# Kernel tuning notes

Hardware: AMD Instinct MI355X
Metric: run time of the kernel (lower is better)

Reference implementation:

```python
import jax, jax.numpy as jnp
import numpy as np

N, E, D_IN, D, H = 50000, 600000, 128, 128, 128
NEG_SLOPE = 0.2  # PyG GATConv default


def setup_inputs() -> dict:
    key = jax.random.key(0)
    ks = jax.random.split(key, 10)
    s = 1.0 / np.sqrt(D)
    return {
        "x": jax.random.normal(ks[0], (N, D_IN), jnp.float32),
        "edge_index": jax.random.randint(ks[1], (2, E), 0, N, jnp.int64),
        "h": jax.random.normal(ks[2], (1, N, H), jnp.float32),
        "c": jax.random.normal(ks[3], (1, N, H), jnp.float32),
        "W": jax.random.normal(ks[4], (D_IN, D), jnp.float32) * s,
        "att_src": jax.random.normal(ks[5], (D,), jnp.float32) * s,
        "att_dst": jax.random.normal(ks[6], (D,), jnp.float32) * s,
        "bias_gat": jnp.zeros((D,), jnp.float32),
        "W_ih": jax.random.normal(ks[7], (4 * H, D), jnp.float32) * s,
        "W_hh": jax.random.normal(ks[8], (4 * H, H), jnp.float32) * s,
    }


def _gat_conv(x, edge_index, W, att_src, att_dst, bias_gat):
    n = x.shape[0]
    xs = x @ W  # [N, D]
    # add self loops (PyG default add_self_loops=True)
    loop = jnp.arange(n, dtype=edge_index.dtype)
    src = jnp.concatenate([edge_index[0], loop])
    dst = jnp.concatenate([edge_index[1], loop])
    a_src = xs @ att_src  # [N]
    a_dst = xs @ att_dst  # [N]
    e = a_src[src] + a_dst[dst]  # [E+N]
    e = jnp.where(e >= 0, e, NEG_SLOPE * e)  # leaky_relu
    # segment softmax over edges grouped by destination node
    e_max = jax.ops.segment_max(e, dst, num_segments=n)
    e_exp = jnp.exp(e - e_max[dst])
    e_sum = jax.ops.segment_sum(e_exp, dst, num_segments=n)
    alpha = e_exp / (e_sum[dst] + 1e-16)  # [E+N]
    out = jax.ops.segment_sum(alpha[:, None] * xs[src], dst, num_segments=n)
    return out + bias_gat


def _lstm_step(x, h0, c0, W_ih, W_hh):
    # torch LSTM gate order: i, f, g, o; bias=False
    gates = x @ W_ih.T + h0 @ W_hh.T  # [N, 4H]
    i, f, g, o = jnp.split(gates, 4, axis=-1)
    i, f, o = jax.nn.sigmoid(i), jax.nn.sigmoid(f), jax.nn.sigmoid(o)
    g = jnp.tanh(g)
    c1 = f * c0 + i * g
    h1 = o * jnp.tanh(c1)
    return h1, c1


def reference(x, edge_index, h, c, W, att_src, att_dst, bias_gat, W_ih, W_hh):
    xb = jnp.tanh(_gat_conv(x, edge_index, W, att_src, att_dst, bias_gat))  # [N, D]
    h1, c1 = _lstm_step(xb, h[0], c[0], W_ih, W_hh)
    # LSTM output for seq_len=1 equals the new hidden state
    return xb * 0 + h1, h1[None], c1[None]
```

## Files before the change

kernel.cpp:

```cpp
#include <hip/hip_runtime.h>
#include <hip/hip_bf16.h>
#include <math.h>

#define NEG 0.2f

typedef float f32x4 __attribute__((ext_vector_type(4)));
typedef short bf16x8 __attribute__((ext_vector_type(8)));

__device__ __forceinline__ float fsig(float x){ return 1.0f/(1.0f+__expf(-x)); }
__device__ __forceinline__ float ftanh(float x){ float e = __expf(2.0f*x); return 1.0f - 2.0f/(e+1.0f); }
__device__ __forceinline__ unsigned short f2bf(float v){
    __hip_bfloat16 b = __float2bfloat16(v);
    return *(unsigned short*)&b;
}
__device__ __forceinline__ bf16x8 pack8(float4 u, float4 v){
    bf16x8 r;
    r[0]=(short)f2bf(u.x); r[1]=(short)f2bf(u.y); r[2]=(short)f2bf(u.z); r[3]=(short)f2bf(u.w);
    r[4]=(short)f2bf(v.x); r[5]=(short)f2bf(v.y); r[6]=(short)f2bf(v.z); r[7]=(short)f2bf(v.w);
    return r;
}
__device__ __forceinline__ bf16x8 asbf(f32x4 v){ union{f32x4 f; bf16x8 h;} u; u.f=v; return u.h; }

__global__ void k_probe(const int* __restrict__ ei, int* __restrict__ flag){
    if(threadIdx.x==0){
        int nz=0;
        for(int i=0;i<64;i++) nz |= ei[2*i+1];
        *flag = (nz==0) ? 1 : 0;
    }
}

__global__ __launch_bounds__(256) void k_wpackx(const float* __restrict__ W,
                                                unsigned short* __restrict__ WPX){
    int f = blockIdx.x*256 + threadIdx.x;
    int l = f&63, ct = (f>>6)&7, ks = f>>9;
    int k0 = ks*32 + (l>>4)*8;
    int col = ct*16 + (l&15);
    #pragma unroll
    for(int j=0;j<8;j++) WPX[(size_t)f*8+j] = f2bf(W[(size_t)(k0+j)*128 + col]);
}

__global__ __launch_bounds__(256) void k_wtpack2(const float* __restrict__ W_ih,
                                                 const float* __restrict__ W_hh,
                                                 unsigned short* __restrict__ WP2){
    int f = blockIdx.x*256 + threadIdx.x;
    int l = f&63, ct = (f>>6)&3, ks = (f>>8)&7, g = f>>11;
    int k0 = ks*32 + (l>>4)*8;
    int col = ct*128 + g*16 + (l&15);
    #pragma unroll
    for(int j=0;j<8;j++){
        int k = k0+j;
        float w = (k<128) ? W_ih[(size_t)col*128+k] : W_hh[(size_t)col*128+(k-128)];
        WP2[(size_t)f*8+j] = f2bf(w);
    }
}

__global__ __launch_bounds__(256,4) void k_gemm_xs4(const float* __restrict__ x,
                                                    const unsigned short* __restrict__ WPX,
                                                    const float* __restrict__ att_s,
                                                    const float* __restrict__ att_d,
                                                    unsigned short* __restrict__ xsb,
                                                    float* __restrict__ a_src,
                                                    float* __restrict__ a_dst,
                                                    int n, int ntiles, int nblk){
    __shared__ unsigned short Bl[16384];
    const int t = threadIdx.x;
    const int w = t>>6, l = t&63;
    {
        const float4* gsrc = (const float4*)WPX;
        float4* ldst = (float4*)Bl;
        #pragma unroll
        for(int i=0;i<8;i++) ldst[t + i*256] = gsrc[t + i*256];
    }
    __syncthreads();
    float asv[8], adv[8];
    #pragma unroll
    for(int ct=0;ct<8;ct++){
        asv[ct] = att_s[ct*16 + (l&15)];
        adv[ct] = att_d[ct*16 + (l&15)];
    }
    for(int rt = blockIdx.x*4 + w; rt < ntiles; rt += nblk*4){
        int arow = rt*16 + (l&15); if(arow>=n) arow = n-1;
        const float* xr = x + (size_t)arow*128 + (l>>4)*8;
        bf16x8 A[4];
        #pragma unroll
        for(int ks=0;ks<4;ks++){
            float4 u = *(const float4*)(xr + ks*32);
            float4 v = *(const float4*)(xr + ks*32 + 4);
            A[ks] = pack8(u,v);
        }
        f32x4 acc[8];
        #pragma unroll
        for(int ct=0;ct<8;ct++) acc[ct] = (f32x4){0.f,0.f,0.f,0.f};
        #pragma unroll
        for(int ks=0;ks<4;ks++){
            #pragma unroll
            for(int ct=0;ct<8;ct++){
                const bf16x8 b = *(const bf16x8*)(Bl + ((ks*8+ct)*64 + l)*8);
                acc[ct] = __builtin_amdgcn_mfma_f32_16x16x32_bf16(A[ks], b, acc[ct], 0,0,0);
            }
        }
        #pragma unroll
        for(int reg=0;reg<4;reg++){
            int row = rt*16 + (l>>4)*4 + reg;
            float ps=0.f, pd=0.f;
            #pragma unroll
            for(int ct=0;ct<8;ct++){ ps += acc[ct][reg]*asv[ct]; pd += acc[ct][reg]*adv[ct]; }
            ps += __shfl_xor(ps,1); pd += __shfl_xor(pd,1);
            ps += __shfl_xor(ps,2); pd += __shfl_xor(pd,2);
            ps += __shfl_xor(ps,4); pd += __shfl_xor(pd,4);
            ps += __shfl_xor(ps,8); pd += __shfl_xor(pd,8);
            if((l&15)==0 && row<n){ a_src[row]=ps; a_dst[row]=pd; }
            if(row<n){
                #pragma unroll
                for(int ct=0;ct<8;ct++)
                    xsb[(size_t)row*128 + ct*16 + (l&15)] = f2bf(acc[ct][reg]);
            }
        }
    }
}

__global__ __launch_bounds__(256) void k_hist(const int* __restrict__ ei,
                                              const int* __restrict__ flag,
                                              int* __restrict__ deg, int E, int EN){
    int e = blockIdx.x*256 + threadIdx.x;
    if(e>=EN) return;
    int dst = (e>=E) ? (e-E) : (*flag ? ei[2*(E+e)] : ei[E+e]);
    atomicAdd(&deg[dst], 1);
}

__global__ __launch_bounds__(256) void k_scan1(const int* __restrict__ deg,
                                               int* __restrict__ bsum, int n){
    __shared__ int ws[4];
    int b = blockIdx.x, t = threadIdx.x;
    int i = b*512 + t*2;
    int s = 0;
    if(i<n)   s += deg[i];
    if(i+1<n) s += deg[i+1];
    for(int off=32;off;off>>=1) s += __shfl_xor(s,off);
    if((t&63)==0) ws[t>>6]=s;
    __syncthreads();
    if(t==0) bsum[b]=ws[0]+ws[1]+ws[2]+ws[3];
}

__global__ void k_scan2(int* __restrict__ bsum, int* __restrict__ rowptr,
                        int nb, int n, int EN){
    int t = threadIdx.x;
    int v0 = (t<nb)    ? bsum[t]    : 0;
    int v1 = (64+t<nb) ? bsum[64+t] : 0;
    int x = v0;
    for(int d=1; d<64; d<<=1){ int y=__shfl_up(x,d); if(t>=d) x+=y; }
    int tot0 = __shfl(x,63);
    int x1 = v1;
    for(int d=1; d<64; d<<=1){ int y=__shfl_up(x1,d); if(t>=d) x1+=y; }
    if(t<nb)    bsum[t]    = x - v0;
    if(64+t<nb) bsum[64+t] = tot0 + x1 - v1;
    if(t==0) rowptr[n]=EN;
}

__global__ __launch_bounds__(256) void k_scan3(const int* __restrict__ deg,
                                               const int* __restrict__ bsum,
                                               int* __restrict__ rowptr,
                                               int* __restrict__ cursor, int n){
    __shared__ int wsum[4];
    int b = blockIdx.x, t = threadIdx.x;
    int i = b*512 + t*2;
    int d0 = (i<n)?deg[i]:0, d1 = (i+1<n)?deg[i+1]:0;
    int s = d0+d1;
    int x = s;
    int lane = t&63, wv = t>>6;
    for(int dd=1; dd<64; dd<<=1){ int y=__shfl_up(x,dd); if(lane>=dd) x+=y; }
    if(lane==63) wsum[wv]=x;
    __syncthreads();
    int woff=0;
    for(int w=0;w<wv;w++) woff += wsum[w];
    int ex = bsum[b] + woff + x - s;
    if(i<n)   { rowptr[i]  =ex;    cursor[i]  =ex;    }
    if(i+1<n) { rowptr[i+1]=ex+d0; cursor[i+1]=ex+d0; }
}

__global__ __launch_bounds__(256) void k_fill(const int* __restrict__ ei,
                                              const int* __restrict__ flag,
                                              int* __restrict__ cursor,
                                              int* __restrict__ csr_src, int E, int EN){
    int e = blockIdx.x*256 + threadIdx.x;
    if(e>=EN) return;
    int src,dst;
    if(e>=E){ src=dst=e-E; }
    else if(*flag){ src = ei[2*e]; dst = ei[2*(E+e)]; }
    else         { src = ei[e];   dst = ei[E+e]; }
    int pos = atomicAdd(&cursor[dst], 1);
    csr_src[pos] = src;
}

__global__ __launch_bounds__(256) void k_agg3(const int* __restrict__ rowptr,
                                              const int* __restrict__ csr_src,
                                              const float* __restrict__ a_src,
                                              const float* __restrict__ a_dst,
                                              const unsigned int* __restrict__ xsb32,
                                              const float* __restrict__ bg,
                                              const float* __restrict__ h0,
                                              unsigned short* __restrict__ xh, int n){
    const int wv = threadIdx.x>>6, l = threadIdx.x&63;
    const int dst = blockIdx.x*4 + wv;
    if(dst>=n) return;
    const int beg = rowptr[dst], end = rowptr[dst+1];
    const float ad = a_dst[dst];
    float ax=0.f, ay=0.f, psum=0.f;
    int j = beg;
    for(; j+4<=end; j+=4){
        int s0=csr_src[j], s1=csr_src[j+1], s2=csr_src[j+2], s3=csr_src[j+3];
        float e0=a_src[s0]+ad, e1=a_src[s1]+ad, e2=a_src[s2]+ad, e3=a_src[s3]+ad;
        unsigned k0=xsb32[(size_t)s0*64+l], k1=xsb32[(size_t)s1*64+l];
        unsigned k2=xsb32[(size_t)s2*64+l], k3=xsb32[(size_t)s3*64+l];
        e0 = e0>=0.f?e0:NEG*e0; e1 = e1>=0.f?e1:NEG*e1;
        e2 = e2>=0.f?e2:NEG*e2; e3 = e3>=0.f?e3:NEG*e3;
        float p0=__expf(e0), p1=__expf(e1), p2=__expf(e2), p3=__expf(e3);
        psum += p0+p1+p2+p3;
        ax += p0*__uint_as_float(k0<<16) + p1*__uint_as_float(k1<<16)
            + p2*__uint_as_float(k2<<16) + p3*__uint_as_float(k3<<16);
        ay += p0*__uint_as_float(k0&0xffff0000u) + p1*__uint_as_float(k1&0xffff0000u)
            + p2*__uint_as_float(k2&0xffff0000u) + p3*__uint_as_float(k3&0xffff0000u);
    }
    for(; j<end; ++j){
        int s = csr_src[j];
        float sv = a_src[s]+ad;
        sv = sv>=0.f ? sv : NEG*sv;
        float p = __expf(sv);
        psum += p;
        unsigned pk = xsb32[(size_t)s*64 + l];
        ax += p*__uint_as_float(pk<<16);
        ay += p*__uint_as_float(pk & 0xffff0000u);
    }
    const float inv = 1.0f/(psum + 1e-16f);
    float t0 = ftanh(ax*inv + bg[2*l]);
    float t1 = ftanh(ay*inv + bg[2*l+1]);
    unsigned int pk = (unsigned)f2bf(t0) | ((unsigned)f2bf(t1)<<16);
    unsigned int* xr = (unsigned int*)(xh + (size_t)dst*256);
    xr[l] = pk;
    float2 hv = *(const float2*)(h0 + (size_t)dst*128 + 2*l);
    xr[64 + l] = (unsigned)f2bf(hv.x) | ((unsigned)f2bf(hv.y)<<16);
}

__global__ __launch_bounds__(256,2) void k_lstm7(const unsigned short* __restrict__ xh,
                                                 const unsigned short* __restrict__ WP2,
                                                 const float* __restrict__ c0,
                                                 float* __restrict__ out,
                                                 int n, int ntiles, int wstride){
    const int t = threadIdx.x;
    const int w = t>>6, l = t&63;
    const int wid = blockIdx.x*4 + w;
    const int g = wid & 7, wgi = wid >> 3;
    const unsigned short* wp = WP2 + (size_t)g*16384;
    f32x4 B[32];
    #pragma unroll
    for(int f=0;f<32;f++) B[f] = *(const f32x4*)(wp + (size_t)(f*64 + l)*8);
    #pragma unroll
    for(int f=0;f<32;f++) asm volatile("" : "+v"(B[f]));
    const size_t nn = (size_t)n*128;
    const int col = g*16 + (l&15);
    int rt = wgi;
    if(rt >= ntiles) return;
    bf16x8 A[8]; float cc[4];
    {
        int arow = rt*16 + (l&15); if(arow>=n) arow=n-1;
        const unsigned short* ar = xh + (size_t)arow*256 + (l>>4)*8;
        #pragma unroll
        for(int ks=0;ks<8;ks++) A[ks] = *(const bf16x8*)(ar + ks*32);
        int rbase = rt*16 + (l>>4)*4;
        #pragma unroll
        for(int r=0;r<4;r++){ int rr=rbase+r; if(rr>=n) rr=n-1; cc[r]=c0[(size_t)rr*128+col]; }
    }
    while(rt < ntiles){
        const int rtn = rt + wstride;
        bf16x8 A2[8]; float cc2[4];
        if(rtn < ntiles){
            int arow = rtn*16 + (l&15); if(arow>=n) arow=n-1;
            const unsigned short* ar = xh + (size_t)arow*256 + (l>>4)*8;
            #pragma unroll
            for(int ks=0;ks<8;ks++) A2[ks] = *(const bf16x8*)(ar + ks*32);
            int rbase = rtn*16 + (l>>4)*4;
            #pragma unroll
            for(int r=0;r<4;r++){ int rr=rbase+r; if(rr>=n) rr=n-1; cc2[r]=c0[(size_t)rr*128+col]; }
        }
        f32x4 acc[4];
        #pragma unroll
        for(int ct=0;ct<4;ct++) acc[ct] = (f32x4){0.f,0.f,0.f,0.f};
        #pragma unroll
        for(int ks=0;ks<8;ks++){
            #pragma unroll
            for(int ct=0;ct<4;ct++)
                acc[ct] = __builtin_amdgcn_mfma_f32_16x16x32_bf16(A[ks], asbf(B[ks*4+ct]), acc[ct], 0,0,0);
        }
        #pragma unroll
        for(int reg=0;reg<4;reg++){
            int row = rt*16 + (l>>4)*4 + reg;
            if(row>=n) continue;
            float gi=acc[0][reg], gf=acc[1][reg], gg=acc[2][reg], go=acc[3][reg];
            float c1v = fsig(gf)*cc[reg] + fsig(gi)*ftanh(gg);
            float h1v = fsig(go)*ftanh(c1v);
            out[(size_t)row*128+col]        = h1v;
            out[nn + (size_t)row*128+col]   = h1v;
            out[2*nn + (size_t)row*128+col] = c1v;
        }
        rt = rtn;
        if(rt < ntiles){
            #pragma unroll
            for(int ks=0;ks<8;ks++) A[ks] = A2[ks];
            #pragma unroll
            for(int r=0;r<4;r++) cc[r] = cc2[r];
        }
    }
}

extern "C" void kernel_launch(void* const* d_in, const int* in_sizes, int n_in,
                              void* d_out, int out_size, void* d_ws, size_t ws_size,
                              hipStream_t stream) {
    const float* x      = (const float*)d_in[0];
    const int*   ei     = (const int*)  d_in[1];
    const float* h      = (const float*)d_in[2];
    const float* c      = (const float*)d_in[3];
    const float* W      = (const float*)d_in[4];
    const float* atts   = (const float*)d_in[5];
    const float* attd   = (const float*)d_in[6];
    const float* bias   = (const float*)d_in[7];
    const float* W_ih   = (const float*)d_in[8];
    const float* W_hh   = (const float*)d_in[9];
    float* out = (float*)d_out;

    const int n  = in_sizes[0]/128;
    const int E  = in_sizes[1]/2;
    const int EN = E + n;
    const int NB = (n + 511)/512;
    const int ntiles = (n + 15)/16;
    const int n2 = ntiles*16;

    unsigned short* xsb = (unsigned short*)d_ws;
    unsigned short* xh  = xsb + (size_t)n*128;
    unsigned short* WP2 = xh + (size_t)n2*256;
    unsigned short* WPX = WP2 + 131072;
    float* a_src = (float*)(WPX + 16384);
    float* a_dst = a_src + n;
    int*   deg    = (int*)(a_dst + n);
    int*   rowptr = deg + n;
    int*   cursor = rowptr + n + 1;
    int*   bsum   = cursor + n;
    int*   csr_src= bsum + 128;
    int*   flag   = csr_src + EN;

    hipMemsetAsync(deg, 0, (size_t)n*sizeof(int), stream);
    k_probe<<<1,64,0,stream>>>(ei, flag);
    k_wpackx<<<8,256,0,stream>>>(W, WPX);
    k_wtpack2<<<64,256,0,stream>>>(W_ih, W_hh, WP2);
    k_gemm_xs4<<<512,256,0,stream>>>(x, WPX, atts, attd, xsb, a_src, a_dst, n, ntiles, 512);
    k_hist<<<(EN+255)/256,256,0,stream>>>(ei,flag,deg,E,EN);
    k_scan1<<<NB,256,0,stream>>>(deg,bsum,n);
    k_scan2<<<1,64,0,stream>>>(bsum,rowptr,NB,n,EN);
    k_scan3<<<NB,256,0,stream>>>(deg,bsum,rowptr,cursor,n);
    k_fill<<<(EN+255)/256,256,0,stream>>>(ei,flag,cursor,csr_src,E,EN);
    k_agg3<<<(n+3)/4,256,0,stream>>>(rowptr,csr_src,a_src,a_dst,(const unsigned int*)xsb,bias,h,xh,n);
    k_lstm7<<<1024,256,0,stream>>>(xh, WP2, c, out, n, ntiles, 512);
}
```

Measured before the change: 196.8 us.

## Hold xs weights in registers, unroll aggregation by eight, use nontemporal LSTM stores

The xs GEMM no longer stages the packed W in LDS. Each wave loads all 32 B fragments into registers, and the kernel launches twice as many blocks with a lower occupancy hint, which removes LDS reads and the block barrier. The edge aggregation loop is unrolled from 4 to 8 edges so more gathers are in flight per wave. The LSTM output writes become nontemporal stores to avoid polluting the cache. The costs are higher register pressure in the GEMM, which lowers occupancy, and more register use in the aggregation kernel.

```diff
diff --git a/kernel.cpp b/kernel.cpp
--- a/kernel.cpp
+++ b/kernel.cpp
@@ -54,31 +54,26 @@
     }
 }
 
-__global__ __launch_bounds__(256,4) void k_gemm_xs4(const float* __restrict__ x,
+__global__ __launch_bounds__(256,2) void k_gemm_xs3(const float* __restrict__ x,
                                                     const unsigned short* __restrict__ WPX,
                                                     const float* __restrict__ att_s,
                                                     const float* __restrict__ att_d,
                                                     unsigned short* __restrict__ xsb,
                                                     float* __restrict__ a_src,
                                                     float* __restrict__ a_dst,
-                                                    int n, int ntiles, int nblk){
-    __shared__ unsigned short Bl[16384];
-    const int t = threadIdx.x;
-    const int w = t>>6, l = t&63;
-    {
-        const float4* gsrc = (const float4*)WPX;
-        float4* ldst = (float4*)Bl;
-        #pragma unroll
-        for(int i=0;i<8;i++) ldst[t + i*256] = gsrc[t + i*256];
-    }
-    __syncthreads();
+                                                    int n, int ntiles, int nwaves){
+    const int w = threadIdx.x>>6, l = threadIdx.x&63;
+    const int wid = blockIdx.x*4 + w;
+    bf16x8 B[32];
+    #pragma unroll
+    for(int f=0;f<32;f++) B[f] = *(const bf16x8*)(WPX + (size_t)(f*64 + l)*8);
     float asv[8], adv[8];
     #pragma unroll
     for(int ct=0;ct<8;ct++){
         asv[ct] = att_s[ct*16 + (l&15)];
         adv[ct] = att_d[ct*16 + (l&15)];
     }
-    for(int rt = blockIdx.x*4 + w; rt < ntiles; rt += nblk*4){
+    for(int rt = wid; rt < ntiles; rt += nwaves){
         int arow = rt*16 + (l&15); if(arow>=n) arow = n-1;
         const float* xr = x + (size_t)arow*128 + (l>>4)*8;
         bf16x8 A[4];
@@ -94,10 +89,8 @@
         #pragma unroll
         for(int ks=0;ks<4;ks++){
             #pragma unroll
-            for(int ct=0;ct<8;ct++){
-                const bf16x8 b = *(const bf16x8*)(Bl + ((ks*8+ct)*64 + l)*8);
-                acc[ct] = __builtin_amdgcn_mfma_f32_16x16x32_bf16(A[ks], b, acc[ct], 0,0,0);
-            }
+            for(int ct=0;ct<8;ct++)
+                acc[ct] = __builtin_amdgcn_mfma_f32_16x16x32_bf16(A[ks], B[ks*8+ct], acc[ct], 0,0,0);
         }
         #pragma unroll
         for(int reg=0;reg<4;reg++){
@@ -207,19 +200,28 @@
     const float ad = a_dst[dst];
     float ax=0.f, ay=0.f, psum=0.f;
     int j = beg;
-    for(; j+4<=end; j+=4){
-        int s0=csr_src[j], s1=csr_src[j+1], s2=csr_src[j+2], s3=csr_src[j+3];
+    for(; j+8<=end; j+=8){
+        int s0=csr_src[j],   s1=csr_src[j+1], s2=csr_src[j+2], s3=csr_src[j+3];
+        int s4=csr_src[j+4], s5=csr_src[j+5], s6=csr_src[j+6], s7=csr_src[j+7];
         float e0=a_src[s0]+ad, e1=a_src[s1]+ad, e2=a_src[s2]+ad, e3=a_src[s3]+ad;
+        float e4=a_src[s4]+ad, e5=a_src[s5]+ad, e6=a_src[s6]+ad, e7=a_src[s7]+ad;
         unsigned k0=xsb32[(size_t)s0*64+l], k1=xsb32[(size_t)s1*64+l];
         unsigned k2=xsb32[(size_t)s2*64+l], k3=xsb32[(size_t)s3*64+l];
-        e0 = e0>=0.f?e0:NEG*e0; e1 = e1>=0.f?e1:NEG*e1;
-        e2 = e2>=0.f?e2:NEG*e2; e3 = e3>=0.f?e3:NEG*e3;
+        unsigned k4=xsb32[(size_t)s4*64+l], k5=xsb32[(size_t)s5*64+l];
+        unsigned k6=xsb32[(size_t)s6*64+l], k7=xsb32[(size_t)s7*64+l];
+        e0=e0>=0.f?e0:NEG*e0; e1=e1>=0.f?e1:NEG*e1; e2=e2>=0.f?e2:NEG*e2; e3=e3>=0.f?e3:NEG*e3;
+        e4=e4>=0.f?e4:NEG*e4; e5=e5>=0.f?e5:NEG*e5; e6=e6>=0.f?e6:NEG*e6; e7=e7>=0.f?e7:NEG*e7;
         float p0=__expf(e0), p1=__expf(e1), p2=__expf(e2), p3=__expf(e3);
-        psum += p0+p1+p2+p3;
+        float p4=__expf(e4), p5=__expf(e5), p6=__expf(e6), p7=__expf(e7);
+        psum += (p0+p1+p2+p3)+(p4+p5+p6+p7);
         ax += p0*__uint_as_float(k0<<16) + p1*__uint_as_float(k1<<16)
-            + p2*__uint_as_float(k2<<16) + p3*__uint_as_float(k3<<16);
+            + p2*__uint_as_float(k2<<16) + p3*__uint_as_float(k3<<16)
+            + p4*__uint_as_float(k4<<16) + p5*__uint_as_float(k5<<16)
+            + p6*__uint_as_float(k6<<16) + p7*__uint_as_float(k7<<16);
         ay += p0*__uint_as_float(k0&0xffff0000u) + p1*__uint_as_float(k1&0xffff0000u)
-            + p2*__uint_as_float(k2&0xffff0000u) + p3*__uint_as_float(k3&0xffff0000u);
+            + p2*__uint_as_float(k2&0xffff0000u) + p3*__uint_as_float(k3&0xffff0000u)
+            + p4*__uint_as_float(k4&0xffff0000u) + p5*__uint_as_float(k5&0xffff0000u)
+            + p6*__uint_as_float(k6&0xffff0000u) + p7*__uint_as_float(k7&0xffff0000u);
     }
     for(; j<end; ++j){
         int s = csr_src[j];
@@ -241,7 +243,7 @@
     xr[64 + l] = (unsigned)f2bf(hv.x) | ((unsigned)f2bf(hv.y)<<16);
 }
 
-__global__ __launch_bounds__(256,2) void k_lstm7(const unsigned short* __restrict__ xh,
+__global__ __launch_bounds__(256,2) void k_lstm8(const unsigned short* __restrict__ xh,
                                                  const unsigned short* __restrict__ WP2,
                                                  const float* __restrict__ c0,
                                                  float* __restrict__ out,
@@ -298,9 +300,9 @@
             float gi=acc[0][reg], gf=acc[1][reg], gg=acc[2][reg], go=acc[3][reg];
             float c1v = fsig(gf)*cc[reg] + fsig(gi)*ftanh(gg);
             float h1v = fsig(go)*ftanh(c1v);
-            out[(size_t)row*128+col]        = h1v;
-            out[nn + (size_t)row*128+col]   = h1v;
-            out[2*nn + (size_t)row*128+col] = c1v;
+            __builtin_nontemporal_store(h1v, &out[(size_t)row*128+col]);
+            __builtin_nontemporal_store(h1v, &out[nn + (size_t)row*128+col]);
+            __builtin_nontemporal_store(c1v, &out[2*nn + (size_t)row*128+col]);
         }
         rt = rtn;
         if(rt < ntiles){
@@ -351,12 +353,12 @@
     k_probe<<<1,64,0,stream>>>(ei, flag);
     k_wpackx<<<8,256,0,stream>>>(W, WPX);
     k_wtpack2<<<64,256,0,stream>>>(W_ih, W_hh, WP2);
-    k_gemm_xs4<<<512,256,0,stream>>>(x, WPX, atts, attd, xsb, a_src, a_dst, n, ntiles, 512);
+    k_gemm_xs3<<<1024,256,0,stream>>>(x, WPX, atts, attd, xsb, a_src, a_dst, n, ntiles, 4096);
     k_hist<<<(EN+255)/256,256,0,stream>>>(ei,flag,deg,E,EN);
     k_scan1<<<NB,256,0,stream>>>(deg,bsum,n);
     k_scan2<<<1,64,0,stream>>>(bsum,rowptr,NB,n,EN);
     k_scan3<<<NB,256,0,stream>>>(deg,bsum,rowptr,cursor,n);
     k_fill<<<(EN+255)/256,256,0,stream>>>(ei,flag,cursor,csr_src,E,EN);
     k_agg3<<<(n+3)/4,256,0,stream>>>(rowptr,csr_src,a_src,a_dst,(const unsigned int*)xsb,bias,h,xh,n);
-    k_lstm7<<<1024,256,0,stream>>>(xh, WP2, c, out, n, ntiles, 512);
-}
+    k_lstm8<<<1024,256,0,stream>>>(xh, WP2, c, out, n, ntiles, 512);
+}
```

New measurement: 180.4 us. 1.09x faster.
